# Kernel tuning notes

Measured on AMD Instinct MI355X. Metric: run time of the kernel, lower is better.

Reference implementation:

```python
import jax, jax.numpy as jnp
import numpy as np

D_MODEL = 1024
D_FF = 4096
NUM_EXPERTS = 8
TOP_K = 2


def setup_inputs() -> dict:
    key = jax.random.key(0)
    ks = jax.random.split(key, 8)
    s_in = 1.0 / np.sqrt(D_MODEL)
    s_ff = 1.0 / np.sqrt(D_FF)
    x = jax.random.normal(ks[0], (2, 2048, D_MODEL), dtype=jnp.float32)
    Wg = jax.random.uniform(ks[1], (D_MODEL, NUM_EXPERTS), minval=-s_in, maxval=s_in, dtype=jnp.float32)
    bg = jax.random.uniform(ks[2], (NUM_EXPERTS,), minval=-s_in, maxval=s_in, dtype=jnp.float32)
    W1 = jax.random.uniform(ks[3], (NUM_EXPERTS, D_MODEL, D_FF), minval=-s_in, maxval=s_in, dtype=jnp.float32)
    b1 = jax.random.uniform(ks[4], (NUM_EXPERTS, D_FF), minval=-s_in, maxval=s_in, dtype=jnp.float32)
    W2 = jax.random.uniform(ks[5], (NUM_EXPERTS, D_FF, D_MODEL), minval=-s_ff, maxval=s_ff, dtype=jnp.float32)
    b2 = jax.random.uniform(ks[6], (NUM_EXPERTS, D_MODEL), minval=-s_ff, maxval=s_ff, dtype=jnp.float32)
    return {"x": x, "Wg": Wg, "bg": bg, "W1": W1, "b1": b1, "W2": W2, "b2": b2}


def reference(x, Wg, bg, W1, b1, W2, b2):
    # Gating: softmax over experts, top-k, renormalize
    gate_logits = jnp.einsum('bsd,de->bse', x, Wg) + bg
    gate_probs = jax.nn.softmax(gate_logits, axis=-1)
    topk_probs, topk_idx = jax.lax.top_k(gate_probs, TOP_K)
    topk_probs = topk_probs / jnp.sum(topk_probs, axis=-1, keepdims=True)
    # Per-token combine weights over experts [B,S,E] (top-k indices are unique)
    onehot = jax.nn.one_hot(topk_idx, NUM_EXPERTS, dtype=x.dtype)  # [B,S,K,E]
    weights = jnp.einsum('bske,bsk->bse', onehot, topk_probs)
    # Dense per-expert FFN (exact GELU matches torch nn.GELU default)
    h = jnp.einsum('bsd,edf->bsef', x, W1) + b1  # [B,S,E,Dff]
    h = jax.nn.gelu(h, approximate=False)
    y = jnp.einsum('bsef,efd->bsed', h, W2) + b2  # [B,S,E,D]
    return jnp.einsum('bsed,bse->bsd', y, weights)
```

## Files before the change

### kernel.cpp

```cpp
#include <hip/hip_runtime.h>
#include <hip/hip_bf16.h>
#include <math.h>

#define D_MODEL 1024
#define D_FF    4096
#define NE      8
#define NTOK    4096
#define MAXTOK  4096

#define MAXROWS 10240
#define MAXMT   40

typedef __attribute__((ext_vector_type(8))) short short8;
typedef __attribute__((ext_vector_type(4))) float f32x4;

#define WS_CNT     0
#define WS_OFFA    128
#define WS_TOKIDS  1024
#define WS_TOKW    (WS_TOKIDS + NE*MAXTOK*4)
#define WS_ROWTOK  (WS_TOKW + NE*MAXTOK*4)
#define WS_ROWW    (WS_ROWTOK + MAXROWS*4)
#define WS_TOKEXP  (WS_ROWW + MAXROWS*4)

#define WS_H       524288
#define WS_W1T     (WS_H   + (size_t)MAXROWS*D_FF*2)
#define WS_XG      (WS_W1T + (size_t)NE*D_MODEL*D_FF*2)
#define WS_W2T     (WS_XG  + (size_t)MAXROWS*D_MODEL*2)
#define WS_NEED_A  (WS_W2T + (size_t)NE*D_MODEL*D_FF*2)

__device__ __forceinline__ ushort f2b(float v) {
    __hip_bfloat16 b = __float2bfloat16(v);
    return *reinterpret_cast<ushort*>(&b);
}

__device__ __forceinline__ float gelu_f(float v) {
    float z = fabsf(v) * 0.70710678118654752f;
    float t = 1.0f / (1.0f + 0.3275911f * z);
    float p = t * (0.254829592f + t * (-0.284496736f + t * (1.421413741f + t * (-1.453152027f + t * 1.061405429f))));
    float er = 1.0f - p * __expf(-z * z);
    float s = (v >= 0.0f) ? er : -er;
    return 0.5f * v * (1.0f + s);
}

__device__ __forceinline__ int xcd_swz(int orig, int nwg) {
    int q = nwg >> 3, r = nwg & 7;
    int xcd = orig & 7, pos = orig >> 3;
    return (xcd < r ? xcd * (q + 1) : r * (q + 1) + (xcd - r) * q) + pos;
}

__device__ __forceinline__ int swz_pos(int sub, int row) {
    int kh = sub >> 2, jj = sub & 3;
    int q = (jj + ((row >> 1) & 3)) & 3;
    return kh * 32 + q * 8;
}

__global__ __launch_bounds__(256) void gating_kernel(
    const float* __restrict__ x, const float* __restrict__ Wg, const float* __restrict__ bg,
    int* __restrict__ cnt, int* __restrict__ tok_ids, float* __restrict__ tok_w,
    int* __restrict__ tokexp)
{
    __shared__ float s_wg[D_MODEL * NE];
    int tid = threadIdx.x;
    for (int i = tid; i < D_MODEL * NE; i += 256) s_wg[i] = Wg[i];
    __syncthreads();

    int t = blockIdx.x * 256 + tid;
    float acc[NE];
    #pragma unroll
    for (int e = 0; e < NE; ++e) acc[e] = bg[e];
    const float* xr = x + (size_t)t * D_MODEL;
    for (int d = 0; d < D_MODEL; d += 4) {
        float4 xv = *reinterpret_cast<const float4*>(xr + d);
        #pragma unroll
        for (int e = 0; e < NE; ++e) {
            acc[e] += xv.x * s_wg[(d + 0) * NE + e];
            acc[e] += xv.y * s_wg[(d + 1) * NE + e];
            acc[e] += xv.z * s_wg[(d + 2) * NE + e];
            acc[e] += xv.w * s_wg[(d + 3) * NE + e];
        }
    }
    int i0 = 0;
    #pragma unroll
    for (int e = 1; e < NE; ++e) if (acc[e] > acc[i0]) i0 = e;
    int i1 = (i0 == 0) ? 1 : 0;
    #pragma unroll
    for (int e = 0; e < NE; ++e) if (e != i0 && acc[e] > acc[i1]) i1 = e;
    float e1 = __expf(acc[i1] - acc[i0]);
    float inv = 1.0f / (1.0f + e1);
    float w0 = inv, w1 = e1 * inv;

    int p0 = atomicAdd(&cnt[i0], 1);
    tok_ids[i0 * MAXTOK + p0] = t;  tok_w[i0 * MAXTOK + p0] = w0;
    tokexp[t * 2 + 0] = i0 * MAXTOK + p0;
    int p1 = atomicAdd(&cnt[i1], 1);
    tok_ids[i1 * MAXTOK + p1] = t;  tok_w[i1 * MAXTOK + p1] = w1;
    tokexp[t * 2 + 1] = i1 * MAXTOK + p1;
}

__global__ void scan256_kernel(const int* __restrict__ cnt, int* __restrict__ off) {
    if (threadIdx.x == 0) {
        int acc = 0;
        for (int e = 0; e < NE; ++e) { off[e] = acc; acc += ((cnt[e] + 255) & ~255); }
        off[NE] = acc;
    }
}

__global__ __launch_bounds__(256) void gather_kernel(
    const float* __restrict__ x, const int* __restrict__ cnt, const int* __restrict__ off,
    const int* __restrict__ tok_ids, const float* __restrict__ tok_w,
    ushort* __restrict__ Xg, int* __restrict__ rowtok, float* __restrict__ roww)
{
    int e = blockIdx.y;
    int npad = off[e + 1] - off[e];
    int r0 = blockIdx.x * 128;
    if (r0 >= npad) return;
    int n = cnt[e];
    int base = off[e];
    for (int idx = threadIdx.x; idx < 128 * 128; idx += 256) {
        int r = r0 + (idx >> 7);
        int s = idx & 127;
        int R = base + r;
        int tok = -1;
        float4 v0 = {0, 0, 0, 0}, v1 = {0, 0, 0, 0};
        if (r < n) {
            tok = tok_ids[e * MAXTOK + r];
            const float4* src = (const float4*)(x + (size_t)tok * D_MODEL + s * 8);
            v0 = src[0]; v1 = src[1];
        }
        ushort o[8];
        o[0] = f2b(v0.x); o[1] = f2b(v0.y); o[2] = f2b(v0.z); o[3] = f2b(v0.w);
        o[4] = f2b(v1.x); o[5] = f2b(v1.y); o[6] = f2b(v1.z); o[7] = f2b(v1.w);
        int c = s >> 3, sub = s & 7;
        *(uint4*)(Xg + (size_t)R * D_MODEL + c * 64 + swz_pos(sub, R)) = *(const uint4*)o;
        if (s == 0) {
            rowtok[R] = tok;
            roww[R] = (tok >= 0) ? tok_w[e * MAXTOK + r] : 0.0f;
        }
    }
}

__global__ __launch_bounds__(256) void wconv_kernel(
    const float* __restrict__ src, ushort* __restrict__ dst, int K, int N)
{
    __shared__ float st[64][65];
    int e = blockIdx.z;
    int n0 = blockIdx.x * 64;
    int k0 = blockIdx.y * 64;
    const float* s = src + (size_t)e * K * N;
    ushort* d = dst + (size_t)e * N * K;
    for (int i = threadIdx.x; i < 4096; i += 256) {
        int kr = i >> 6, nc = i & 63;
        st[kr][nc] = s[(size_t)(k0 + kr) * N + n0 + nc];
    }
    __syncthreads();
    int c = k0 >> 6;
    #pragma unroll
    for (int it = 0; it < 2; ++it) {
        int v = threadIdx.x + it * 256;
        int nl = v >> 3, sub = v & 7;
        ushort o[8];
        #pragma unroll
        for (int j = 0; j < 8; ++j) o[j] = f2b(st[sub * 8 + j][nl]);
        *(uint4*)(d + (size_t)(n0 + nl) * K + c * 64 + swz_pos(sub, n0 + nl)) = *(const uint4*)o;
    }
}


#define STAGE_U(gbase, gstride, ktw, kh, slot, breg) { \
    _Pragma("unroll") \
    for (int l = 0; l < 2; ++l) { \
        int flat = l * 512 + tid; int row_ = flat >> 2, q_ = flat & 3; \
        __builtin_amdgcn_global_load_lds( \
            (const __attribute__((address_space(1))) void*)((gbase) + (size_t)row_ * (gstride) + (ktw) * 64 + (kh) * 32 + q_ * 8), \
            (__attribute__((address_space(3))) void*)(smem + (breg) + (slot) * 16384 + (kh) * 8192 + flat * 8), 16, 0, 0); \
    } }

#define PHASE(s, kh, mh, DO_B, STAGE_CODE, VMC) { \
    const ushort* As_ = smem + (s) * 16384 + (kh) * 8192; \
    const ushort* Bs_ = smem + 32768 + (s) * 16384 + (kh) * 8192; \
    if (DO_B) { \
        _Pragma("unroll") \
        for (int n = 0; n < 4; ++n) { \
            int br = wcn + n * 16; \
            int q = (jj + ((br >> 1) & 3)) & 3; \
            bfr[n] = *(const short8*)(Bs_ + br * 32 + q * 8); \
        } } \
    short8 afr[4]; \
    _Pragma("unroll") \
    for (int m = 0; m < 4; ++m) { \
        int ar = wrm + (mh) * 64 + m * 16; \
        int q = (jj + ((ar >> 1) & 3)) & 3; \
        afr[m] = *(const short8*)(As_ + ar * 32 + q * 8); \
    } \
    STAGE_CODE; \
    __builtin_amdgcn_s_barrier(); \
    asm volatile("s_waitcnt lgkmcnt(0)" ::: "memory"); \
    __builtin_amdgcn_s_setprio(1); \
    _Pragma("unroll") \
    for (int m = 0; m < 4; ++m) \
        _Pragma("unroll") \
        for (int n = 0; n < 4; ++n) \
            acc[(mh) * 4 + m][n] = __builtin_amdgcn_mfma_f32_16x16x32_bf16(afr[m], bfr[n], acc[(mh) * 4 + m][n], 0, 0, 0); \
    __builtin_amdgcn_s_setprio(0); \
    if (VMC) asm volatile("s_waitcnt vmcnt(4)" ::: "memory"); \
    __builtin_amdgcn_s_barrier(); \
}

template<bool GELU>
__global__ __launch_bounds__(512, 2) void gemm8(
    const ushort* __restrict__ Aall, const ushort* __restrict__ Ball,
    const float* __restrict__ bias, const int* __restrict__ off,
    ushort* __restrict__ Hout, float* __restrict__ Yout)
{
    __shared__ ushort smem[65536];
    constexpr int LDA  = GELU ? D_MODEL : D_FF;
    constexpr int NDIM = GELU ? D_FF : D_MODEL;
    constexpr int NKS  = GELU ? 1 : 2;
    constexpr int NK   = LDA / (64 * NKS);
    constexpr int NT   = NDIM >> 8;
    constexpr int PER  = NT * NKS;

    int wid = xcd_swz(blockIdx.x, MAXMT * PER);
    int mt = wid / PER; int rr = wid % PER;
    int nt = rr % NT;   int ks = rr / NT;
    int row0 = mt << 8;
    if (row0 >= off[NE]) return;
    int e = 0;
    #pragma unroll
    for (int i = 1; i < NE; ++i) if (off[i] <= row0) e = i;
    int nb0 = nt << 8;
    int ktbase = ks * NK;

    int tid = threadIdx.x;
    int lane = tid & 63, wave = tid >> 6;
    int wr = wave >> 2, wc = wave & 3;
    int jj = lane >> 4;
    int wrm = wr * 128 + (lane & 15);
    int wcn = wc * 64 + (lane & 15);

    const ushort* Ab = Aall + (size_t)row0 * LDA;
    const ushort* Bb = Ball + ((size_t)e * NDIM + nb0) * LDA;

    f32x4 acc[8][4];
    #pragma unroll
    for (int m = 0; m < 8; ++m)
        #pragma unroll
        for (int n = 0; n < 4; ++n)
            acc[m][n] = (f32x4){0.f, 0.f, 0.f, 0.f};

    STAGE_U(Ab, LDA, ktbase, 0, 0, 0);
    STAGE_U(Bb, LDA, ktbase, 0, 0, 32768);
    STAGE_U(Ab, LDA, ktbase, 1, 0, 0);
    STAGE_U(Bb, LDA, ktbase, 1, 0, 32768);
    asm volatile("s_waitcnt vmcnt(4)" ::: "memory");
    __builtin_amdgcn_s_barrier();

    short8 bfr[4];
    for (int kt = 0; kt < NK; ++kt) {
        int s = kt & 1, sn = s ^ 1;
        int ktn = (kt + 1 == NK) ? 0 : kt + 1;
        int kta = ktbase + ktn;
        PHASE(s, 0, 0, 1, STAGE_U(Ab, LDA, kta, 0, sn, 0), 0);
        PHASE(s, 0, 1, 0, STAGE_U(Bb, LDA, kta, 0, sn, 32768), 1);
        PHASE(s, 1, 0, 1, STAGE_U(Ab, LDA, kta, 1, sn, 0), 0);
        PHASE(s, 1, 1, 0, STAGE_U(Bb, LDA, kta, 1, sn, 32768), 1);
    }
    asm volatile("s_waitcnt vmcnt(0)" ::: "memory");
    __syncthreads();

    if (GELU) {
        const float* be = bias + (size_t)e * NDIM + nb0;
        #pragma unroll
        for (int n = 0; n < 4; ++n) {
            int cl = wc * 64 + n * 16 + (lane & 15);
            float bv = be[cl];
            int c4 = cl >> 6, sub = (cl >> 3) & 7, el = cl & 7;
            #pragma unroll
            for (int m = 0; m < 8; ++m) {
                int rb = wr * 128 + m * 16 + (lane >> 4) * 4;
                #pragma unroll
                for (int qq = 0; qq < 4; ++qq) {
                    int row = rb + qq;
                    float v = gelu_f(acc[m][n][qq] + bv);
                    smem[row * 256 + c4 * 64 + swz_pos(sub, row) + el] = f2b(v);
                }
            }
        }
        __syncthreads();
        #pragma unroll
        for (int it = 0; it < 16; ++it) {
            int flat = it * 512 + tid;
            int row = flat >> 5, g = flat & 31;
            *(uint4*)(Hout + (size_t)(row0 + row) * NDIM + nb0 + g * 8) = *(const uint4*)(smem + flat * 8);
        }
    } else {
        const float* be = bias + (size_t)e * NDIM + nb0;
        float* Yb = Yout + (size_t)ks * MAXROWS * NDIM;
        #pragma unroll
        for (int n = 0; n < 4; ++n) {
            int cl = wc * 64 + n * 16 + (lane & 15);
            float bv = (ks == 0) ? be[cl] : 0.0f;
            #pragma unroll
            for (int m = 0; m < 8; ++m) {
                int rb = wr * 128 + m * 16 + (lane >> 4) * 4;
                #pragma unroll
                for (int qq = 0; qq < 4; ++qq)
                    Yb[(size_t)(row0 + rb + qq) * NDIM + nb0 + cl] = acc[m][n][qq] + bv;
            }
        }
    }
}

__global__ __launch_bounds__(256) void combine_kernel(
    const float* __restrict__ Y, const int* __restrict__ off,
    const int* __restrict__ tokexp, const float* __restrict__ tok_w,
    float* __restrict__ out, int nks)
{
    int t = blockIdx.x;
    int pos0 = tokexp[2 * t], pos1 = tokexp[2 * t + 1];
    int e0 = pos0 >> 12, p0 = pos0 & (MAXTOK - 1);
    int e1 = pos1 >> 12, p1 = pos1 & (MAXTOK - 1);
    size_t R0 = off[e0] + p0, R1 = off[e1] + p1;
    float w0 = tok_w[pos0], w1 = tok_w[pos1];
    int c = threadIdx.x * 4;
    float y0x = 0, y0y = 0, y0z = 0, y0w = 0;
    float y1x = 0, y1y = 0, y1z = 0, y1w = 0;
    for (int s = 0; s < nks; ++s) {
        const float* Ys = Y + (size_t)s * MAXROWS * D_MODEL;
        float4 a = *(const float4*)(Ys + R0 * D_MODEL + c);
        float4 b = *(const float4*)(Ys + R1 * D_MODEL + c);
        y0x += a.x; y0y += a.y; y0z += a.z; y0w += a.w;
        y1x += b.x; y1y += b.y; y1z += b.z; y1w += b.w;
    }
    float4 o;
    o.x = w0 * y0x + w1 * y1x;
    o.y = w0 * y0y + w1 * y1y;
    o.z = w0 * y0z + w1 * y1z;
    o.w = w0 * y0w + w1 * y1w;
    *(float4*)(out + (size_t)t * D_MODEL + c) = o;
}

#define TM      32
#define FFC     128
#define KSTEP   64

__global__ __launch_bounds__(512) void ffn_kernel(
    const float* __restrict__ x,
    const float* __restrict__ W1, const float* __restrict__ b1,
    const float* __restrict__ W2, const float* __restrict__ b2,
    const int* __restrict__ cnt, const int* __restrict__ tok_ids, const float* __restrict__ tok_w,
    float* __restrict__ out)
{
    int e = blockIdx.y;
    int n = cnt[e];
    int t0 = blockIdx.x * TM;
    if (t0 >= n) return;
    int tid = threadIdx.x;

    __shared__ int   s_tok[TM];
    __shared__ float s_w[TM];
    __shared__ float s_x[TM][KSTEP];
    __shared__ float s_w1[KSTEP][FFC];
    __shared__ float s_h[TM][FFC];

    if (tid < TM) {
        int idx = t0 + tid;
        s_tok[tid] = (idx < n) ? tok_ids[e * MAXTOK + idx] : -1;
        s_w[tid]   = (idx < n) ? tok_w[e * MAXTOK + idx] : 0.0f;
    }
    __syncthreads();

    float acc[TM][2];
    #pragma unroll
    for (int i = 0; i < TM; ++i) { acc[i][0] = 0.0f; acc[i][1] = 0.0f; }

    const float* W1e = W1 + (size_t)e * D_MODEL * D_FF;
    const float* W2e = W2 + (size_t)e * D_FF * D_MODEL;
    const float* b1e = b1 + (size_t)e * D_FF;

    int ffl = (tid & 63) * 2;
    int g   = tid >> 6;

    int fb0 = blockIdx.z * (D_FF / 2);
    for (int fb = fb0; fb < fb0 + D_FF / 2; fb += FFC) {
        float bv0 = b1e[fb + ffl], bv1 = b1e[fb + ffl + 1];
        float hacc[4][2];
        #pragma unroll
        for (int j = 0; j < 4; ++j) { hacc[j][0] = bv0; hacc[j][1] = bv1; }

        for (int kb = 0; kb < D_MODEL; kb += KSTEP) {
            #pragma unroll
            for (int r = 0; r < 4; ++r) {
                int i = tid + 512 * r;
                int row = i >> 6, col = i & 63;
                int tok = s_tok[row];
                s_x[row][col] = (tok >= 0) ? x[(size_t)tok * D_MODEL + kb + col] : 0.0f;
            }
            #pragma unroll
            for (int r = 0; r < 16; ++r) {
                int i = tid + 512 * r;
                int row = i >> 7, col = i & 127;
                s_w1[row][col] = W1e[(size_t)(kb + row) * D_FF + fb + col];
            }
            __syncthreads();
            #pragma unroll 8
            for (int kk = 0; kk < KSTEP; ++kk) {
                float2 wv = *reinterpret_cast<const float2*>(&s_w1[kk][ffl]);
                #pragma unroll
                for (int j = 0; j < 4; ++j) {
                    float xv = s_x[g * 4 + j][kk];
                    hacc[j][0] += xv * wv.x;
                    hacc[j][1] += xv * wv.y;
                }
            }
            __syncthreads();
        }
        #pragma unroll
        for (int j = 0; j < 4; ++j) {
            #pragma unroll
            for (int p = 0; p < 2; ++p) {
                float v = hacc[j][p];
                v = 0.5f * v * (1.0f + erff(v * 0.70710678118654752f));
                s_h[g * 4 + j][ffl + p] = v;
            }
        }
        __syncthreads();
        for (int ff = 0; ff < FFC; ++ff) {
            const float* w2row = W2e + (size_t)(fb + ff) * D_MODEL;
            float wc0 = w2row[tid], wc1 = w2row[tid + 512];
            #pragma unroll
            for (int tt = 0; tt < TM; ++tt) {
                float hv = s_h[tt][ff];
                acc[tt][0] += hv * wc0;
                acc[tt][1] += hv * wc1;
            }
        }
        __syncthreads();
    }

    float bc0 = b2[(size_t)e * D_MODEL + tid];
    float bc1 = b2[(size_t)e * D_MODEL + tid + 512];
    if (blockIdx.z != 0) { bc0 = 0.0f; bc1 = 0.0f; }
    #pragma unroll
    for (int tt = 0; tt < TM; ++tt) {
        int tok = s_tok[tt];
        if (tok >= 0) {
            float w = s_w[tt];
            atomicAdd(&out[(size_t)tok * D_MODEL + tid],       w * (acc[tt][0] + bc0));
            atomicAdd(&out[(size_t)tok * D_MODEL + tid + 512], w * (acc[tt][1] + bc1));
        }
    }
}

extern "C" void kernel_launch(void* const* d_in, const int* in_sizes, int n_in,
                              void* d_out, int out_size, void* d_ws, size_t ws_size,
                              hipStream_t stream) {
    const float* x  = (const float*)d_in[0];
    const float* Wg = (const float*)d_in[1];
    const float* bg = (const float*)d_in[2];
    const float* W1 = (const float*)d_in[3];
    const float* b1 = (const float*)d_in[4];
    const float* W2 = (const float*)d_in[5];
    const float* b2 = (const float*)d_in[6];
    float* out = (float*)d_out;

    char* ws = (char*)d_ws;
    int*    cnt     = (int*)(ws + WS_CNT);
    int*    offp    = (int*)(ws + WS_OFFA);
    int*    tok_ids = (int*)(ws + WS_TOKIDS);
    float*  tok_w   = (float*)(ws + WS_TOKW);
    int*    rowtok  = (int*)(ws + WS_ROWTOK);
    float*  roww    = (float*)(ws + WS_ROWW);
    int*    tokexp  = (int*)(ws + WS_TOKEXP);

    hipMemsetAsync(cnt, 0, NE * sizeof(int), stream);
    gating_kernel<<<NTOK / 256, 256, 0, stream>>>(x, Wg, bg, cnt, tok_ids, tok_w, tokexp);

    if (ws_size >= WS_NEED_A) {
        ushort* Hb  = (ushort*)(ws + WS_H);
        ushort* W1T = (ushort*)(ws + WS_W1T);
        ushort* Xg  = (ushort*)(ws + WS_XG);
        ushort* W2T = (ushort*)(ws + WS_W2T);
        float*  Y   = (float*)(ws + WS_W1T);
        const int nks = 2;

        scan256_kernel<<<1, 64, 0, stream>>>(cnt, offp);
        wconv_kernel<<<dim3(D_FF / 64, D_MODEL / 64, NE), 256, 0, stream>>>(W1, W1T, D_MODEL, D_FF);
        wconv_kernel<<<dim3(D_MODEL / 64, D_FF / 64, NE), 256, 0, stream>>>(W2, W2T, D_FF, D_MODEL);
        gather_kernel<<<dim3(32, NE), 256, 0, stream>>>(x, cnt, offp, tok_ids, tok_w, Xg, rowtok, roww);
        gemm8<true><<<MAXMT * 16, 512, 0, stream>>>(Xg, W1T, b1, offp, Hb, nullptr);
        gemm8<false><<<MAXMT * 8, 512, 0, stream>>>(Hb, W2T, b2, offp, nullptr, Y);
        combine_kernel<<<NTOK, 256, 0, stream>>>(Y, offp, tokexp, tok_w, out, nks);
    } else {
        hipMemsetAsync(out, 0, (size_t)out_size * sizeof(float), stream);
        dim3 grid(MAXTOK / TM, NE, 2);
        ffn_kernel<<<grid, 512, 0, stream>>>(x, W1, b1, W2, b2, cnt, tok_ids, tok_w, out);
    }
}
```

Baseline: 479.0 us.

## Restructure grouped GEMM into 8-phase half-tile pipeline with XOR swizzle

The grouped bf16 GEMM main loop is reorganized so each k-tile of 64 is split into row-halves of A and B. The loop runs eight phases per two k-tiles, each computing one 128x128 quadrant and staging one half-tile, which keeps more global loads in flight (vmcnt 6/8) and drops the explicit lgkmcnt wait. LDS layout switches from a 32-element rotated swizzle to a full 64-element row with XOR swizzle, applied consistently in weight conversion, gather and the epilogue. The two weight-conversion launches are merged into one. The deeper pipeline raises register pressure and scheduling complexity, and the cross-phase buffer reuse could cause hazards.

```diff
diff --git a/kernel.cpp b/kernel.cpp
--- a/kernel.cpp
+++ b/kernel.cpp
@@ -49,9 +49,7 @@
 }
 
 __device__ __forceinline__ int swz_pos(int sub, int row) {
-    int kh = sub >> 2, jj = sub & 3;
-    int q = (jj + ((row >> 1) & 3)) & 3;
-    return kh * 32 + q * 8;
+    return (sub ^ (row & 7)) * 8;
 }
 
 __global__ __launch_bounds__(256) void gating_kernel(
@@ -139,15 +137,19 @@
     }
 }
 
-__global__ __launch_bounds__(256) void wconv_kernel(
-    const float* __restrict__ src, ushort* __restrict__ dst, int K, int N)
+__global__ __launch_bounds__(256) void wconv_all(
+    const float* __restrict__ W1, const float* __restrict__ W2,
+    ushort* __restrict__ W1T, ushort* __restrict__ W2T)
 {
     __shared__ float st[64][65];
-    int e = blockIdx.z;
-    int n0 = blockIdx.x * 64;
-    int k0 = blockIdx.y * 64;
-    const float* s = src + (size_t)e * K * N;
-    ushort* d = dst + (size_t)e * N * K;
+    int z = blockIdx.y;
+    const float* s; ushort* d; int K, N;
+    if (z < 8) { s = W1 + (size_t)z * D_MODEL * D_FF;       d = W1T + (size_t)z * D_MODEL * D_FF; K = D_MODEL; N = D_FF; }
+    else       { s = W2 + (size_t)(z - 8) * D_FF * D_MODEL; d = W2T + (size_t)(z - 8) * D_FF * D_MODEL; K = D_FF; N = D_MODEL; }
+    int nblk = N >> 6;
+    int bx = blockIdx.x;
+    int n0 = (bx % nblk) * 64;
+    int k0 = (bx / nblk) * 64;
     for (int i = threadIdx.x; i < 4096; i += 256) {
         int kr = i >> 6, nc = i & 63;
         st[kr][nc] = s[(size_t)(k0 + kr) * N + n0 + nc];
@@ -166,48 +168,50 @@
 }
 
 
-#define STAGE_U(gbase, gstride, ktw, kh, slot, breg) { \
+#define STAGEH(gb, gstride, ldsoff, half, kt) { \
     _Pragma("unroll") \
     for (int l = 0; l < 2; ++l) { \
-        int flat = l * 512 + tid; int row_ = flat >> 2, q_ = flat & 3; \
+        int flat = l * 512 + tid; int lr_ = flat >> 3, s_ = flat & 7; \
         __builtin_amdgcn_global_load_lds( \
-            (const __attribute__((address_space(1))) void*)((gbase) + (size_t)row_ * (gstride) + (ktw) * 64 + (kh) * 32 + q_ * 8), \
-            (__attribute__((address_space(3))) void*)(smem + (breg) + (slot) * 16384 + (kh) * 8192 + flat * 8), 16, 0, 0); \
+            (const __attribute__((address_space(1))) void*)((gb) + (size_t)((half) * 128 + lr_) * (gstride) + (size_t)(kt) * 64 + s_ * 8), \
+            (__attribute__((address_space(3))) void*)(smem + (ldsoff) + flat * 8), 16, 0, 0); \
     } }
 
-#define PHASE(s, kh, mh, DO_B, STAGE_CODE, VMC) { \
-    const ushort* As_ = smem + (s) * 16384 + (kh) * 8192; \
-    const ushort* Bs_ = smem + 32768 + (s) * 16384 + (kh) * 8192; \
-    if (DO_B) { \
-        _Pragma("unroll") \
-        for (int n = 0; n < 4; ++n) { \
-            int br = wcn + n * 16; \
-            int q = (jj + ((br >> 1) & 3)) & 3; \
-            bfr[n] = *(const short8*)(Bs_ + br * 32 + q * 8); \
-        } } \
-    short8 afr[4]; \
+#define PH(slot, mh, nh, STAGE_CODE) { \
+    const ushort* Ah_ = smem + ((slot) * 2 + (mh)) * 8192; \
+    const ushort* Bh_ = smem + 32768 + ((slot) * 2 + (nh)) * 8192; \
+    short8 av[4][2], bv[2][2]; \
     _Pragma("unroll") \
     for (int m = 0; m < 4; ++m) { \
-        int ar = wrm + (mh) * 64 + m * 16; \
-        int q = (jj + ((ar >> 1) & 3)) & 3; \
-        afr[m] = *(const short8*)(As_ + ar * 32 + q * 8); \
+        int lr = wr64 + m * 16 + l15; \
+        _Pragma("unroll") \
+        for (int k2 = 0; k2 < 2; ++k2) \
+            av[m][k2] = *(const short8*)(Ah_ + lr * 64 + ((k2 * 4 + jj) ^ (lr & 7)) * 8); \
+    } \
+    _Pragma("unroll") \
+    for (int n = 0; n < 2; ++n) { \
+        int br = wc32 + n * 16 + l15; \
+        _Pragma("unroll") \
+        for (int k2 = 0; k2 < 2; ++k2) \
+            bv[n][k2] = *(const short8*)(Bh_ + br * 64 + ((k2 * 4 + jj) ^ (br & 7)) * 8); \
     } \
     STAGE_CODE; \
     __builtin_amdgcn_s_barrier(); \
-    asm volatile("s_waitcnt lgkmcnt(0)" ::: "memory"); \
     __builtin_amdgcn_s_setprio(1); \
     _Pragma("unroll") \
     for (int m = 0; m < 4; ++m) \
         _Pragma("unroll") \
-        for (int n = 0; n < 4; ++n) \
-            acc[(mh) * 4 + m][n] = __builtin_amdgcn_mfma_f32_16x16x32_bf16(afr[m], bfr[n], acc[(mh) * 4 + m][n], 0, 0, 0); \
+        for (int n = 0; n < 2; ++n) { \
+            acc[(mh) * 4 + m][(nh) * 2 + n] = __builtin_amdgcn_mfma_f32_16x16x32_bf16(av[m][0], bv[n][0], acc[(mh) * 4 + m][(nh) * 2 + n], 0, 0, 0); \
+            acc[(mh) * 4 + m][(nh) * 2 + n] = __builtin_amdgcn_mfma_f32_16x16x32_bf16(av[m][1], bv[n][1], acc[(mh) * 4 + m][(nh) * 2 + n], 0, 0, 0); \
+        } \
     __builtin_amdgcn_s_setprio(0); \
-    if (VMC) asm volatile("s_waitcnt vmcnt(4)" ::: "memory"); \
+    asm volatile("s_waitcnt vmcnt(6)" ::: "memory"); \
     __builtin_amdgcn_s_barrier(); \
 }
 
 template<bool GELU>
-__global__ __launch_bounds__(512, 2) void gemm8(
+__global__ __launch_bounds__(512, 2) void gemm8p(
     const ushort* __restrict__ Aall, const ushort* __restrict__ Ball,
     const float* __restrict__ bias, const int* __restrict__ off,
     ushort* __restrict__ Hout, float* __restrict__ Yout)
@@ -216,7 +220,8 @@
     constexpr int LDA  = GELU ? D_MODEL : D_FF;
     constexpr int NDIM = GELU ? D_FF : D_MODEL;
     constexpr int NKS  = GELU ? 1 : 2;
-    constexpr int NK   = LDA / (64 * NKS);
+    constexpr int NKT  = LDA / (64 * NKS);
+    constexpr int NIT  = NKT / 2;
     constexpr int NT   = NDIM >> 8;
     constexpr int PER  = NT * NKS;
 
@@ -229,14 +234,13 @@
     #pragma unroll
     for (int i = 1; i < NE; ++i) if (off[i] <= row0) e = i;
     int nb0 = nt << 8;
-    int ktbase = ks * NK;
+    int ktb = ks * NKT;
 
     int tid = threadIdx.x;
     int lane = tid & 63, wave = tid >> 6;
     int wr = wave >> 2, wc = wave & 3;
-    int jj = lane >> 4;
-    int wrm = wr * 128 + (lane & 15);
-    int wcn = wc * 64 + (lane & 15);
+    int jj = lane >> 4, l15 = lane & 15;
+    int wr64 = wr * 64, wc32 = wc * 32;
 
     const ushort* Ab = Aall + (size_t)row0 * LDA;
     const ushort* Bb = Ball + ((size_t)e * NDIM + nb0) * LDA;
@@ -248,22 +252,27 @@
         for (int n = 0; n < 4; ++n)
             acc[m][n] = (f32x4){0.f, 0.f, 0.f, 0.f};
 
-    STAGE_U(Ab, LDA, ktbase, 0, 0, 0);
-    STAGE_U(Bb, LDA, ktbase, 0, 0, 32768);
-    STAGE_U(Ab, LDA, ktbase, 1, 0, 0);
-    STAGE_U(Bb, LDA, ktbase, 1, 0, 32768);
-    asm volatile("s_waitcnt vmcnt(4)" ::: "memory");
+    STAGEH(Ab, LDA, 0,             0, ktb + 0);
+    STAGEH(Bb, LDA, 32768,         0, ktb + 0);
+    STAGEH(Ab, LDA, 8192,          1, ktb + 0);
+    STAGEH(Bb, LDA, 32768 + 8192,  1, ktb + 0);
+    STAGEH(Ab, LDA, 16384,         0, ktb + 1);
+    STAGEH(Bb, LDA, 32768 + 16384, 0, ktb + 1);
+    asm volatile("s_waitcnt vmcnt(8)" ::: "memory");
     __builtin_amdgcn_s_barrier();
 
-    short8 bfr[4];
-    for (int kt = 0; kt < NK; ++kt) {
-        int s = kt & 1, sn = s ^ 1;
-        int ktn = (kt + 1 == NK) ? 0 : kt + 1;
-        int kta = ktbase + ktn;
-        PHASE(s, 0, 0, 1, STAGE_U(Ab, LDA, kta, 0, sn, 0), 0);
-        PHASE(s, 0, 1, 0, STAGE_U(Bb, LDA, kta, 0, sn, 32768), 1);
-        PHASE(s, 1, 0, 1, STAGE_U(Ab, LDA, kta, 1, sn, 0), 0);
-        PHASE(s, 1, 1, 0, STAGE_U(Bb, LDA, kta, 1, sn, 32768), 1);
+    for (int it2 = 0; it2 < NIT; ++it2) {
+        int t1  = 2 * it2 + 1;
+        int tn0 = (2 * it2 + 2 == NKT) ? 0 : 2 * it2 + 2;
+        int tn1 = (2 * it2 + 3 >= NKT) ? 1 : 2 * it2 + 3;
+        PH(0, 0, 0, STAGEH(Ab, LDA, 24576,         1, ktb + t1));
+        PH(0, 0, 1, STAGEH(Bb, LDA, 32768 + 24576, 1, ktb + t1));
+        PH(0, 1, 0, STAGEH(Ab, LDA, 0,             0, ktb + tn0));
+        PH(0, 1, 1, STAGEH(Bb, LDA, 32768,         0, ktb + tn0));
+        PH(1, 0, 0, STAGEH(Ab, LDA, 8192,          1, ktb + tn0));
+        PH(1, 0, 1, STAGEH(Bb, LDA, 32768 + 8192,  1, ktb + tn0));
+        PH(1, 1, 0, STAGEH(Ab, LDA, 16384,         0, ktb + tn1));
+        PH(1, 1, 1, STAGEH(Bb, LDA, 32768 + 16384, 0, ktb + tn1));
     }
     asm volatile("s_waitcnt vmcnt(0)" ::: "memory");
     __syncthreads();
@@ -271,17 +280,21 @@
     if (GELU) {
         const float* be = bias + (size_t)e * NDIM + nb0;
         #pragma unroll
-        for (int n = 0; n < 4; ++n) {
-            int cl = wc * 64 + n * 16 + (lane & 15);
-            float bv = be[cl];
-            int c4 = cl >> 6, sub = (cl >> 3) & 7, el = cl & 7;
+        for (int mh = 0; mh < 2; ++mh)
+        #pragma unroll
+        for (int nh = 0; nh < 2; ++nh)
+        #pragma unroll
+        for (int n = 0; n < 2; ++n) {
+            int col = nh * 128 + wc32 + n * 16 + l15;
+            float bv = be[col];
+            int c4 = col >> 6, sub = (col >> 3) & 7, el = col & 7;
             #pragma unroll
-            for (int m = 0; m < 8; ++m) {
-                int rb = wr * 128 + m * 16 + (lane >> 4) * 4;
+            for (int m = 0; m < 4; ++m) {
+                int rb = mh * 128 + wr64 + m * 16 + jj * 4;
                 #pragma unroll
                 for (int qq = 0; qq < 4; ++qq) {
                     int row = rb + qq;
-                    float v = gelu_f(acc[m][n][qq] + bv);
+                    float v = gelu_f(acc[mh * 4 + m][nh * 2 + n][qq] + bv);
                     smem[row * 256 + c4 * 64 + swz_pos(sub, row) + el] = f2b(v);
                 }
             }
@@ -297,15 +310,19 @@
         const float* be = bias + (size_t)e * NDIM + nb0;
         float* Yb = Yout + (size_t)ks * MAXROWS * NDIM;
         #pragma unroll
-        for (int n = 0; n < 4; ++n) {
-            int cl = wc * 64 + n * 16 + (lane & 15);
-            float bv = (ks == 0) ? be[cl] : 0.0f;
+        for (int mh = 0; mh < 2; ++mh)
+        #pragma unroll
+        for (int nh = 0; nh < 2; ++nh)
+        #pragma unroll
+        for (int n = 0; n < 2; ++n) {
+            int col = nh * 128 + wc32 + n * 16 + l15;
+            float bv = (ks == 0) ? be[col] : 0.0f;
             #pragma unroll
-            for (int m = 0; m < 8; ++m) {
-                int rb = wr * 128 + m * 16 + (lane >> 4) * 4;
+            for (int m = 0; m < 4; ++m) {
+                int rb = mh * 128 + wr64 + m * 16 + jj * 4;
                 #pragma unroll
                 for (int qq = 0; qq < 4; ++qq)
-                    Yb[(size_t)(row0 + rb + qq) * NDIM + nb0 + cl] = acc[m][n][qq] + bv;
+                    Yb[(size_t)(row0 + rb + qq) * NDIM + nb0 + col] = acc[mh * 4 + m][nh * 2 + n][qq] + bv;
             }
         }
     }
@@ -485,11 +502,10 @@
         const int nks = 2;
 
         scan256_kernel<<<1, 64, 0, stream>>>(cnt, offp);
-        wconv_kernel<<<dim3(D_FF / 64, D_MODEL / 64, NE), 256, 0, stream>>>(W1, W1T, D_MODEL, D_FF);
-        wconv_kernel<<<dim3(D_MODEL / 64, D_FF / 64, NE), 256, 0, stream>>>(W2, W2T, D_FF, D_MODEL);
+        wconv_all<<<dim3(1024, 16), 256, 0, stream>>>(W1, W2, W1T, W2T);
         gather_kernel<<<dim3(32, NE), 256, 0, stream>>>(x, cnt, offp, tok_ids, tok_w, Xg, rowtok, roww);
-        gemm8<true><<<MAXMT * 16, 512, 0, stream>>>(Xg, W1T, b1, offp, Hb, nullptr);
-        gemm8<false><<<MAXMT * 8, 512, 0, stream>>>(Hb, W2T, b2, offp, nullptr, Y);
+        gemm8p<true><<<MAXMT * 16, 512, 0, stream>>>(Xg, W1T, b1, offp, Hb, nullptr);
+        gemm8p<false><<<MAXMT * 8, 512, 0, stream>>>(Hb, W2T, b2, offp, nullptr, Y);
         combine_kernel<<<NTOK, 256, 0, stream>>>(Y, offp, tokexp, tok_w, out, nks);
     } else {
         hipMemsetAsync(out, 0, (size_t)out_size * sizeof(float), stream);
```

Measured after the change: 486.9 us. Within noise of the previous version (+1.6%).
